# Optimization experiments

Measured on AMD Instinct MI355X. Metric: run time of the kernel, lower is better.

Reference implementation:

```python
import jax, jax.numpy as jnp
import numpy as np

N = 100000
E = 1600000
FEAT = 128
EMB = 64
HID = 64
OUT = 16


def _glorot(key, shape):
    fan_in, fan_out = shape[1], shape[0]
    lim = (6.0 / (fan_in + fan_out)) ** 0.5
    return jax.random.uniform(key, shape, jnp.float32, -lim, lim)


def setup_inputs() -> dict:
    key = jax.random.key(0)
    ks = jax.random.split(key, 16)
    return {
        "x_feat": jax.random.normal(ks[0], (N, FEAT), jnp.float32),
        "x_emb": jax.random.normal(ks[1], (N, 2, EMB), jnp.float32),
        "edge_index": jax.random.randint(ks[2], (2, E), 0, N, jnp.int32),
        # layer 0: SAGEConv(FEAT -> HID), Linear(EMB -> HID)
        "Wl0": _glorot(ks[3], (HID, FEAT)),
        "bl0": jnp.zeros((HID,), jnp.float32),
        "Wr0": _glorot(ks[4], (HID, FEAT)),
        "We0": _glorot(ks[5], (HID, EMB)),
        "be0": jnp.zeros((HID,), jnp.float32),
        # layer 1 (last): SAGEConv(HID -> OUT), Linear(EMB==HID -> OUT)
        "Wl1": _glorot(ks[6], (OUT, HID)),
        "bl1": jnp.zeros((OUT,), jnp.float32),
        "Wr1": _glorot(ks[7], (OUT, HID)),
        "We1": _glorot(ks[8], (OUT, HID)),
        "be1": jnp.zeros((OUT,), jnp.float32),
    }


def _sage_conv(x, edge_index, Wl, bl, Wr):
    # PyG SAGEConv with mean aggregation:
    #   out = lin_l(mean_{j in N(i)} x_j) + lin_r(x_i)
    src, dst = edge_index[0], edge_index[1]
    msg = x[src]                                   # [E, C] gather
    agg = jax.ops.segment_sum(msg, dst, num_segments=N)       # [N, C]
    deg = jax.ops.segment_sum(jnp.ones((E,), x.dtype), dst, num_segments=N)
    agg = agg / jnp.maximum(deg, 1.0)[:, None]     # mean over neighbors
    return agg @ Wl.T + bl + x @ Wr.T


def reference(x_feat, x_emb, edge_index,
              Wl0, bl0, Wr0, We0, be0,
              Wl1, bl1, Wr1, We1, be1):
    # forward(x=(x_feat, x_emb), edge_index=...) path, eval mode (dropout p=0)
    e = x_emb.mean(axis=1)                         # [N, EMB]
    # layer 0 (all but last): relu(sage + linear(emb))
    h = _sage_conv(x_feat, edge_index, Wl0, bl0, Wr0)
    e = e @ We0.T + be0
    h = jax.nn.relu(h + e)
    # last layer: no relu
    h = _sage_conv(h, edge_index, Wl1, bl1, Wr1)
    e = e @ We1.T + be1
    return h + e
```

## Files before the change

### kernel.cpp

```cpp
#include <hip/hip_runtime.h>
#include <hip/hip_bf16.h>
#include <cstddef>

#define NN 100000
#define EE 1600000
#define NPB 128
#define NB  782
#define ECH 4096
#define NCH 391
#define CAP 4096

typedef __attribute__((ext_vector_type(8))) short bf16x8;
typedef __attribute__((ext_vector_type(8))) unsigned short u16x8;
typedef __attribute__((ext_vector_type(4))) float f32x4;

#define YTS 72
#define RTS 68

static inline int ceil_div(int a, int b){ return (a + b - 1) / b; }

__device__ inline unsigned short f2bf(float f){
  union { float f; unsigned u; } v; v.f = f;
  unsigned r = (v.u + 0x7fff + ((v.u >> 16) & 1)) >> 16;
  return (unsigned short)r;
}
__device__ inline float bf2f(unsigned short s){
  union { unsigned u; float f; } v; v.u = ((unsigned)s) << 16;
  return v.f;
}

#define PRE_W (128 * 192)
#define PRE_E (PRE_W + 16 * 64)
#define PRE_B (PRE_E + 16)
#define PRE_C (PRE_B + 64)
#define PRE_N (PRE_C + NB)
__global__ void prep_all_kernel(const float* __restrict__ Wl0, const float* __restrict__ Wr0,
                                const float* __restrict__ We0, const float* __restrict__ bl0,
                                const float* __restrict__ be0, const float* __restrict__ We1,
                                const float* __restrict__ be1,
                                unsigned short* __restrict__ wcat, float* __restrict__ wee,
                                float* __restrict__ b1e, float* __restrict__ bias0,
                                int* __restrict__ cur){
  int idx = blockIdx.x * blockDim.x + threadIdx.x;
  if (idx < PRE_W){
    int n = idx / 192, k = idx % 192;
    float v;
    if (n < 64) v = (k < 128) ? Wl0[n * 128 + k] : 0.f;
    else        v = (k < 128) ? Wr0[(n - 64) * 128 + k] : We0[(n - 64) * 64 + (k - 128)];
    wcat[idx] = f2bf(v);
  } else if (idx < PRE_E){
    int j = idx - PRE_W;
    int i = j >> 6, c = j & 63;
    float s = 0.f;
    for (int k = 0; k < 64; k++) s += We1[i * 64 + k] * We0[k * 64 + c];
    wee[j] = s;
  } else if (idx < PRE_B){
    int i = idx - PRE_E;
    float s = be1[i];
    for (int k = 0; k < 64; k++) s += We1[i * 64 + k] * be0[k];
    b1e[i] = s;
  } else if (idx < PRE_C){
    int i = idx - PRE_B;
    bias0[i] = bl0[i] + be0[i];
  } else if (idx < PRE_N){
    cur[idx - PRE_C] = 0;
  }
}

__global__ void eprep_kernel(const float* __restrict__ xe, unsigned short* __restrict__ eb){
  int g = blockIdx.x * blockDim.x + threadIdx.x;
  if (g >= NN * 8) return;
  int node = g >> 3, q = g & 7;
  float4 a0 = ((const float4*)xe)[(size_t)node * 32 + q * 2];
  float4 a1 = ((const float4*)xe)[(size_t)node * 32 + q * 2 + 1];
  float4 b0 = ((const float4*)xe)[(size_t)node * 32 + 16 + q * 2];
  float4 b1 = ((const float4*)xe)[(size_t)node * 32 + 16 + q * 2 + 1];
  u16x8 o;
  o[0]=f2bf(0.5f*(a0.x+b0.x)); o[1]=f2bf(0.5f*(a0.y+b0.y));
  o[2]=f2bf(0.5f*(a0.z+b0.z)); o[3]=f2bf(0.5f*(a0.w+b0.w));
  o[4]=f2bf(0.5f*(a1.x+b1.x)); o[5]=f2bf(0.5f*(a1.y+b1.y));
  o[6]=f2bf(0.5f*(a1.z+b1.z)); o[7]=f2bf(0.5f*(a1.w+b1.w));
  *(u16x8*)&eb[(size_t)node * 64 + q * 8] = o;
}

__global__ __launch_bounds__(1024) void escatter_kernel(const int* __restrict__ src,
                                                        const int* __restrict__ dst,
                                                        int* __restrict__ cur,
                                                        int* __restrict__ ebkt){
  __shared__ int lh[NB];
  __shared__ int lo[NB];
  const int t = threadIdx.x;
  const int c = blockIdx.x;
  const int e0 = c * ECH;
  int ne = EE - e0; if (ne > ECH) ne = ECH;
  for (int i = t; i < NB; i += 1024) lh[i] = 0;
  __syncthreads();
  int dl[4], sl[4];
  #pragma unroll
  for (int k = 0; k < 4; k++){
    int i = t + k * 1024;
    dl[k] = (i < ne) ? dst[e0 + i] : -1;
    sl[k] = (i < ne) ? src[e0 + i] : 0;
  }
  #pragma unroll
  for (int k = 0; k < 4; k++)
    if (dl[k] >= 0) atomicAdd(&lh[dl[k] >> 7], 1);
  __syncthreads();
  for (int i = t; i < NB; i += 1024){
    int cc = lh[i];
    lo[i] = cc ? atomicAdd(&cur[i], cc) : 0;
    lh[i] = 0;
  }
  __syncthreads();
  #pragma unroll
  for (int k = 0; k < 4; k++){
    if (dl[k] >= 0){
      int d = dl[k], b = d >> 7;
      int r = atomicAdd(&lh[b], 1);
      int p = lo[b] + r;
      if (p < CAP) ebkt[b * CAP + p] = ((d & 127) << 24) | sl[k];
    }
  }
}

__global__ __launch_bounds__(256) void bsort_kernel(
    const int* __restrict__ cur, int* __restrict__ ebkt,
    int* __restrict__ rs, int* __restrict__ deg){
  __shared__ int lraw[CAP];
  __shared__ int lout[CAP];
  __shared__ int lh[NPB];
  __shared__ int loff[NPB];
  __shared__ int lcur[NPB];
  const int t = threadIdx.x;
  const int b = blockIdx.x;
  const int e0 = b * CAP;
  int cnt = cur[b];
  if (cnt > CAP) cnt = CAP;
  for (int i = t; i < NPB; i += 256) lh[i] = 0;
  __syncthreads();
  for (int i = t; i < cnt; i += 256){
    int w = ebkt[e0 + i];
    lraw[i] = w;
    atomicAdd(&lh[((unsigned)w) >> 24], 1);
  }
  __syncthreads();
  {
    int v = (t < NPB) ? lh[t] : 0;
    int s = v;
    for (int off = 1; off < NPB; off <<= 1){
      int x = 0;
      if (t < NPB && t >= off) x = loff[t - off];
      __syncthreads();
      if (t < NPB) loff[t] = s;
      __syncthreads();
      if (t < NPB && t >= off) s += loff[t - off];
      __syncthreads();
    }
    if (t < NPB){ loff[t] = s - v; lcur[t] = s - v; }
  }
  __syncthreads();
  for (int i = t; i < cnt; i += 256){
    int w = lraw[i];
    int d = ((unsigned)w) >> 24;
    int pos = atomicAdd(&lcur[d], 1);
    lout[pos] = w & 0xFFFFFF;
  }
  __syncthreads();
  for (int i = t; i < cnt; i += 256) ebkt[e0 + i] = lout[i];
  if (t < NPB){
    int node = b * NPB + t;
    if (node < NN){
      rs[node]  = e0 + loff[t];
      deg[node] = lh[t];
    }
  }
}

__global__ __launch_bounds__(256, 3) void l0_gemm_kernel(
    const float* __restrict__ xf, const unsigned short* __restrict__ eb,
    const unsigned short* __restrict__ wcat,
    unsigned short* __restrict__ y0g, float* __restrict__ re0g, int M){
  __shared__ unsigned short As[64 * 200];
  __shared__ unsigned short Ys[64 * YTS];
  __shared__ float          Rs[64 * RTS];
  const int t = threadIdx.x;
  const int row0 = blockIdx.x * 64;
  float4 fa[4], fb[4];
  u16x8 ev[2];
  #pragma unroll
  for (int k = 0; k < 4; k++){
    int idx = t + k * 256;
    int r = idx >> 4, o = idx & 15;
    int row = row0 + r;
    if (row < M){
      fa[k] = ((const float4*)xf)[(size_t)row * 32 + o * 2];
      fb[k] = ((const float4*)xf)[(size_t)row * 32 + o * 2 + 1];
    } else {
      fa[k] = make_float4(0.f,0.f,0.f,0.f);
      fb[k] = make_float4(0.f,0.f,0.f,0.f);
    }
  }
  #pragma unroll
  for (int k = 0; k < 2; k++){
    int idx = t + k * 256;
    int r = idx >> 3, q = idx & 7;
    int row = row0 + r;
    u16x8 z = {0,0,0,0,0,0,0,0};
    ev[k] = (row < M) ? *(const u16x8*)&eb[(size_t)row * 64 + q * 8] : z;
  }
  #pragma unroll
  for (int k = 0; k < 4; k++){
    int idx = t + k * 256;
    int r = idx >> 4, o = idx & 15;
    u16x8 ov;
    ov[0]=f2bf(fa[k].x); ov[1]=f2bf(fa[k].y); ov[2]=f2bf(fa[k].z); ov[3]=f2bf(fa[k].w);
    ov[4]=f2bf(fb[k].x); ov[5]=f2bf(fb[k].y); ov[6]=f2bf(fb[k].z); ov[7]=f2bf(fb[k].w);
    *(u16x8*)&As[r * 200 + o * 8] = ov;
  }
  #pragma unroll
  for (int k = 0; k < 2; k++){
    int idx = t + k * 256;
    int r = idx >> 3, q = idx & 7;
    *(u16x8*)&As[r * 200 + 128 + q * 8] = ev[k];
  }
  const int w = t >> 6, l = t & 63;
  const int lm = l & 15, quad = l >> 4;
  bf16x8 bfr0[6], bfr1[6];
  {
    int n0 = w * 16 + lm;
    int n1 = 64 + w * 16 + lm;
    #pragma unroll
    for (int ks = 0; ks < 6; ks++){
      bfr0[ks] = *(const bf16x8*)&wcat[n0 * 192 + ks * 32 + quad * 8];
      bfr1[ks] = *(const bf16x8*)&wcat[n1 * 192 + ks * 32 + quad * 8];
    }
  }
  __syncthreads();
  for (int rg = 0; rg < 4; rg++){
    bf16x8 af[6];
    #pragma unroll
    for (int ks = 0; ks < 6; ks++)
      af[ks] = *(const bf16x8*)&As[(rg * 16 + lm) * 200 + ks * 32 + quad * 8];
    f32x4 acc0 = {0.f, 0.f, 0.f, 0.f};
    f32x4 acc1 = {0.f, 0.f, 0.f, 0.f};
    #pragma unroll
    for (int ks = 0; ks < 6; ks++){
      acc0 = __builtin_amdgcn_mfma_f32_16x16x32_bf16(af[ks], bfr0[ks], acc0, 0, 0, 0);
      acc1 = __builtin_amdgcn_mfma_f32_16x16x32_bf16(af[ks], bfr1[ks], acc1, 0, 0, 0);
    }
    #pragma unroll
    for (int r = 0; r < 4; r++){
      int lrow = rg * 16 + quad * 4 + r;
      Ys[lrow * YTS + w * 16 + lm] = f2bf(acc0[r]);
      Rs[lrow * RTS + w * 16 + lm] = acc1[r];
    }
  }
  __syncthreads();
  #pragma unroll
  for (int k = 0; k < 2; k++){
    int idx = t + k * 256;
    int r = idx >> 3, c8 = idx & 7;
    int grow = row0 + r;
    if (grow < M)
      *(u16x8*)&y0g[(size_t)grow * 64 + c8 * 8] = *(const u16x8*)&Ys[r * YTS + c8 * 8];
  }
  #pragma unroll
  for (int k = 0; k < 4; k++){
    int idx = t + k * 256;
    int r = idx >> 4, c4 = idx & 15;
    int grow = row0 + r;
    if (grow < M)
      *(f32x4*)&re0g[(size_t)grow * 64 + c4 * 4] = *(const f32x4*)&Rs[r * RTS + c4 * 4];
  }
}

__global__ void agg0_kernel(const unsigned short* __restrict__ y0,
                            const float* __restrict__ re0,
                            const float* __restrict__ bias0,
                            const int* __restrict__ rs, const int* __restrict__ deg,
                            const int* __restrict__ ssrc, unsigned short* __restrict__ h){
  int g = blockIdx.x * blockDim.x + threadIdx.x;
  if (g >= NN * 8) return;
  int node = g >> 3, lane = g & 7;
  int start = rs[node], cnt = deg[node];
  float acc[4][8] = {};
  int i = 0;
  for (; i + 8 <= cnt; i += 8){
    int s[8];
    #pragma unroll
    for (int j = 0; j < 8; j++) s[j] = ssrc[start + i + j];
    u16x8 v[8];
    #pragma unroll
    for (int j = 0; j < 8; j++) v[j] = *(const u16x8*)&y0[(size_t)s[j] * 64 + lane * 8];
    #pragma unroll
    for (int j = 0; j < 8; j++)
      #pragma unroll
      for (int k = 0; k < 8; k++) acc[j & 3][k] += bf2f((unsigned short)v[j][k]);
  }
  for (; i < cnt; i++){
    int s = ssrc[start + i];
    u16x8 v = *(const u16x8*)&y0[(size_t)s * 64 + lane * 8];
    #pragma unroll
    for (int k = 0; k < 8; k++) acc[0][k] += bf2f((unsigned short)v[k]);
  }
  float inv = 1.0f / (float)(cnt > 1 ? cnt : 1);
  f32x4 rv0 = *(const f32x4*)&re0[(size_t)node * 64 + lane * 8];
  f32x4 rv1 = *(const f32x4*)&re0[(size_t)node * 64 + lane * 8 + 4];
  float rvv[8] = {rv0[0], rv0[1], rv0[2], rv0[3], rv1[0], rv1[1], rv1[2], rv1[3]};
  float4 ba = ((const float4*)bias0)[lane * 2];
  float4 bb = ((const float4*)bias0)[lane * 2 + 1];
  float bv[8] = {ba.x, ba.y, ba.z, ba.w, bb.x, bb.y, bb.z, bb.w};
  u16x8 o;
  #pragma unroll
  for (int k = 0; k < 8; k++){
    float sum = (acc[0][k] + acc[1][k]) + (acc[2][k] + acc[3][k]);
    float x = sum * inv + rvv[k] + bv[k];
    o[k] = f2bf(x > 0.f ? x : 0.f);
  }
  *(u16x8*)&h[(size_t)node * 64 + lane * 8] = o;
}

__global__ __launch_bounds__(256) void gemm16_dual_kernel(
    const unsigned short* __restrict__ H, const unsigned short* __restrict__ eb,
    const float* __restrict__ Wl1, const float* __restrict__ Wr1,
    const float* __restrict__ wee,
    const float* __restrict__ bl1, const float* __restrict__ b1e,
    unsigned short* __restrict__ Y1, float* __restrict__ Out, int M){
  __shared__ float Hs[64][65];
  __shared__ float Es[64][65];
  __shared__ float Wls[16][65];
  __shared__ float Wrs[16][65];
  __shared__ float Wes[16][65];
  __shared__ float bs[16];
  const int t = threadIdx.x;
  const int row0 = blockIdx.x * 64;
  {
    int j = t >> 4, kq = t & 15;
    float4 a = ((const float4*)Wl1)[j * 16 + kq];
    float4 b = ((const float4*)Wr1)[j * 16 + kq];
    float4 c = ((const float4*)wee)[j * 16 + kq];
    Wls[j][kq*4+0]=a.x; Wls[j][kq*4+1]=a.y; Wls[j][kq*4+2]=a.z; Wls[j][kq*4+3]=a.w;
    Wrs[j][kq*4+0]=b.x; Wrs[j][kq*4+1]=b.y; Wrs[j][kq*4+2]=b.z; Wrs[j][kq*4+3]=b.w;
    Wes[j][kq*4+0]=c.x; Wes[j][kq*4+1]=c.y; Wes[j][kq*4+2]=c.z; Wes[j][kq*4+3]=c.w;
  }
  if (t < 16) bs[t] = bl1[t] + b1e[t];
  for (int idx = t; idx < 64 * 16; idx += 256){
    int n = idx >> 4, kq = idx & 15;
    int row = row0 + n;
    ushort4 hv = make_ushort4(0,0,0,0), evv = make_ushort4(0,0,0,0);
    if (row < M){
      hv  = *(const ushort4*)&H[(size_t)row * 64 + kq * 4];
      evv = *(const ushort4*)&eb[(size_t)row * 64 + kq * 4];
    }
    Hs[n][kq*4+0]=bf2f(hv.x); Hs[n][kq*4+1]=bf2f(hv.y); Hs[n][kq*4+2]=bf2f(hv.z); Hs[n][kq*4+3]=bf2f(hv.w);
    Es[n][kq*4+0]=bf2f(evv.x); Es[n][kq*4+1]=bf2f(evv.y); Es[n][kq*4+2]=bf2f(evv.z); Es[n][kq*4+3]=bf2f(evv.w);
  }
  __syncthreads();
  const int n = t >> 2, jq = t & 3;
  float y[4] = {}, o[4] = {};
  #pragma unroll 4
  for (int k = 0; k < 64; k++){
    float a = Hs[n][k];
    float e = Es[n][k];
    #pragma unroll
    for (int j = 0; j < 4; j++){
      y[j] = fmaf(a, Wls[jq*4 + j][k], y[j]);
      o[j] = fmaf(a, Wrs[jq*4 + j][k], o[j]);
      o[j] = fmaf(e, Wes[jq*4 + j][k], o[j]);
    }
  }
  int row = row0 + n;
  if (row < M){
    ushort4 yb; yb.x = f2bf(y[0]); yb.y = f2bf(y[1]); yb.z = f2bf(y[2]); yb.w = f2bf(y[3]);
    *(ushort4*)&Y1[(size_t)row * 16 + jq * 4] = yb;
    ((float4*)Out)[(size_t)row * 4 + jq] =
        make_float4(o[0] + bs[jq*4+0], o[1] + bs[jq*4+1], o[2] + bs[jq*4+2], o[3] + bs[jq*4+3]);
  }
}

__global__ void agg1_kernel(const unsigned short* __restrict__ y1,
                            const int* __restrict__ rs, const int* __restrict__ deg,
                            const int* __restrict__ ssrc, float* __restrict__ outp){
  int g = blockIdx.x * blockDim.x + threadIdx.x;
  if (g >= NN * 2) return;
  int node = g >> 1, lane = g & 1;
  int start = rs[node], cnt = deg[node];
  float acc[4][8] = {};
  int i = 0;
  for (; i + 8 <= cnt; i += 8){
    int s[8];
    #pragma unroll
    for (int j = 0; j < 8; j++) s[j] = ssrc[start + i + j];
    u16x8 v[8];
    #pragma unroll
    for (int j = 0; j < 8; j++) v[j] = *(const u16x8*)&y1[(size_t)s[j] * 16 + lane * 8];
    #pragma unroll
    for (int j = 0; j < 8; j++)
      #pragma unroll
      for (int k = 0; k < 8; k++) acc[j & 3][k] += bf2f((unsigned short)v[j][k]);
  }
  for (; i < cnt; i++){
    int s = ssrc[start + i];
    u16x8 v = *(const u16x8*)&y1[(size_t)s * 16 + lane * 8];
    #pragma unroll
    for (int k = 0; k < 8; k++) acc[0][k] += bf2f((unsigned short)v[k]);
  }
  float inv = 1.0f / (float)(cnt > 1 ? cnt : 1);
  f32x4 o0 = *(f32x4*)&outp[(size_t)node * 16 + lane * 8];
  f32x4 o1 = *(f32x4*)&outp[(size_t)node * 16 + lane * 8 + 4];
  #pragma unroll
  for (int k = 0; k < 4; k++){
    o0[k] += ((acc[0][k] + acc[1][k]) + (acc[2][k] + acc[3][k])) * inv;
    o1[k] += ((acc[0][k+4] + acc[1][k+4]) + (acc[2][k+4] + acc[3][k+4])) * inv;
  }
  *(f32x4*)&outp[(size_t)node * 16 + lane * 8]     = o0;
  *(f32x4*)&outp[(size_t)node * 16 + lane * 8 + 4] = o1;
}

extern "C" void kernel_launch(void* const* d_in, const int* in_sizes, int n_in,
                              void* d_out, int out_size, void* d_ws, size_t ws_size,
                              hipStream_t stream){
  (void)in_sizes; (void)n_in; (void)out_size; (void)ws_size;
  const float* x_feat = (const float*)d_in[0];
  const float* x_emb  = (const float*)d_in[1];
  const int*   ei     = (const int*)d_in[2];
  const float* Wl0 = (const float*)d_in[3];
  const float* bl0 = (const float*)d_in[4];
  const float* Wr0 = (const float*)d_in[5];
  const float* We0 = (const float*)d_in[6];
  const float* be0 = (const float*)d_in[7];
  const float* Wl1 = (const float*)d_in[8];
  const float* bl1 = (const float*)d_in[9];
  const float* Wr1 = (const float*)d_in[10];
  const float* We1 = (const float*)d_in[11];
  const float* be1 = (const float*)d_in[12];
  float* out = (float*)d_out;

  char* w = (char*)d_ws;
  float* re0          = (float*)w;           w += sizeof(float) * (size_t)NN * 64;
  unsigned short* y0  = (unsigned short*)w;  w += sizeof(unsigned short) * (size_t)NN * 64;
  unsigned short* eb  = (unsigned short*)w;  w += sizeof(unsigned short) * (size_t)NN * 64;
  unsigned short* h   = (unsigned short*)w;  w += sizeof(unsigned short) * (size_t)NN * 64;
  unsigned short* y1  = (unsigned short*)w;  w += sizeof(unsigned short) * (size_t)NN * 16;
  unsigned short* wcat= (unsigned short*)w;  w += sizeof(unsigned short) * 128 * 192;
  float* wee   = (float*)w;                  w += sizeof(float) * 16 * 64;
  float* b1e   = (float*)w;                  w += sizeof(float) * 16;
  float* bias0 = (float*)w;                  w += sizeof(float) * 64;
  int* ebkt    = (int*)w;                    w += sizeof(int) * (size_t)NB * CAP;
  int* cur     = (int*)w;                    w += sizeof(int) * NB;
  int* rs      = (int*)w;                    w += sizeof(int) * NN;
  int* deg     = (int*)w;                    w += sizeof(int) * NN;

  const int* srcp = ei;
  const int* dstp = ei + EE;

  prep_all_kernel<<<ceil_div(PRE_N, 256), 256, 0, stream>>>(
      Wl0, Wr0, We0, bl0, be0, We1, be1, wcat, wee, b1e, bias0, cur);

  escatter_kernel<<<NCH, 1024, 0, stream>>>(srcp, dstp, cur, ebkt);
  bsort_kernel<<<NB, 256, 0, stream>>>(cur, ebkt, rs, deg);

  eprep_kernel<<<ceil_div(NN * 8, 256), 256, 0, stream>>>(x_emb, eb);

  l0_gemm_kernel<<<ceil_div(NN, 64), 256, 0, stream>>>(x_feat, eb, wcat, y0, re0, NN);

  agg0_kernel<<<ceil_div(NN * 8, 256), 256, 0, stream>>>(
      y0, re0, bias0, rs, deg, ebkt, h);

  gemm16_dual_kernel<<<ceil_div(NN, 64), 256, 0, stream>>>(h, eb, Wl1, Wr1, wee,
                                                           bl1, b1e, y1, out, NN);
  agg1_kernel<<<ceil_div(NN * 2, 256), 256, 0, stream>>>(y1, rs, deg, ebkt, out);
}
```

Before: 282.8 us.

## Fuse bucket sort into layer-0 aggregation kernel using shared-memory sorted edges

Removes the separate bucket-sort kernel and performs the per-bucket counting sort inside the layer-0 aggregation kernel, one block per 128-node bucket. Neighbor indices are then read from shared memory instead of global memory, and one launch is saved. The sorted edges, rs and deg are still written out for the layer-1 aggregation. In exchange, the aggregation now runs on only 782 blocks with 32KB of shared memory each, which lowers occupancy and parallelism for the gather-heavy phase.

```diff
diff --git a/kernel.cpp b/kernel.cpp
--- a/kernel.cpp
+++ b/kernel.cpp
@@ -123,59 +123,6 @@
   }
 }
 
-__global__ __launch_bounds__(256) void bsort_kernel(
-    const int* __restrict__ cur, int* __restrict__ ebkt,
-    int* __restrict__ rs, int* __restrict__ deg){
-  __shared__ int lraw[CAP];
-  __shared__ int lout[CAP];
-  __shared__ int lh[NPB];
-  __shared__ int loff[NPB];
-  __shared__ int lcur[NPB];
-  const int t = threadIdx.x;
-  const int b = blockIdx.x;
-  const int e0 = b * CAP;
-  int cnt = cur[b];
-  if (cnt > CAP) cnt = CAP;
-  for (int i = t; i < NPB; i += 256) lh[i] = 0;
-  __syncthreads();
-  for (int i = t; i < cnt; i += 256){
-    int w = ebkt[e0 + i];
-    lraw[i] = w;
-    atomicAdd(&lh[((unsigned)w) >> 24], 1);
-  }
-  __syncthreads();
-  {
-    int v = (t < NPB) ? lh[t] : 0;
-    int s = v;
-    for (int off = 1; off < NPB; off <<= 1){
-      int x = 0;
-      if (t < NPB && t >= off) x = loff[t - off];
-      __syncthreads();
-      if (t < NPB) loff[t] = s;
-      __syncthreads();
-      if (t < NPB && t >= off) s += loff[t - off];
-      __syncthreads();
-    }
-    if (t < NPB){ loff[t] = s - v; lcur[t] = s - v; }
-  }
-  __syncthreads();
-  for (int i = t; i < cnt; i += 256){
-    int w = lraw[i];
-    int d = ((unsigned)w) >> 24;
-    int pos = atomicAdd(&lcur[d], 1);
-    lout[pos] = w & 0xFFFFFF;
-  }
-  __syncthreads();
-  for (int i = t; i < cnt; i += 256) ebkt[e0 + i] = lout[i];
-  if (t < NPB){
-    int node = b * NPB + t;
-    if (node < NN){
-      rs[node]  = e0 + loff[t];
-      deg[node] = lh[t];
-    }
-  }
-}
-
 __global__ __launch_bounds__(256, 3) void l0_gemm_kernel(
     const float* __restrict__ xf, const unsigned short* __restrict__ eb,
     const unsigned short* __restrict__ wcat,
@@ -274,50 +221,98 @@
   }
 }
 
-__global__ void agg0_kernel(const unsigned short* __restrict__ y0,
-                            const float* __restrict__ re0,
-                            const float* __restrict__ bias0,
-                            const int* __restrict__ rs, const int* __restrict__ deg,
-                            const int* __restrict__ ssrc, unsigned short* __restrict__ h){
-  int g = blockIdx.x * blockDim.x + threadIdx.x;
-  if (g >= NN * 8) return;
-  int node = g >> 3, lane = g & 7;
-  int start = rs[node], cnt = deg[node];
-  float acc[4][8] = {};
-  int i = 0;
-  for (; i + 8 <= cnt; i += 8){
-    int s[8];
-    #pragma unroll
-    for (int j = 0; j < 8; j++) s[j] = ssrc[start + i + j];
-    u16x8 v[8];
-    #pragma unroll
-    for (int j = 0; j < 8; j++) v[j] = *(const u16x8*)&y0[(size_t)s[j] * 64 + lane * 8];
-    #pragma unroll
-    for (int j = 0; j < 8; j++)
+__global__ __launch_bounds__(256) void agg0_kernel(
+    const unsigned short* __restrict__ y0, const float* __restrict__ re0,
+    const float* __restrict__ bias0, const int* __restrict__ cur,
+    int* __restrict__ ebkt, int* __restrict__ rs, int* __restrict__ deg,
+    unsigned short* __restrict__ h){
+  __shared__ int lraw[CAP];
+  __shared__ int lsrt[CAP];
+  __shared__ int lh[NPB];
+  __shared__ int loff[NPB];
+  __shared__ int lcur[NPB];
+  const int t = threadIdx.x;
+  const int b = blockIdx.x;
+  const int e0 = b * CAP;
+  int cnt = cur[b]; if (cnt > CAP) cnt = CAP;
+  for (int i = t; i < NPB; i += 256) lh[i] = 0;
+  __syncthreads();
+  for (int i = t; i < cnt; i += 256){
+    int w = ebkt[e0 + i];
+    lraw[i] = w;
+    atomicAdd(&lh[((unsigned)w) >> 24], 1);
+  }
+  __syncthreads();
+  {
+    int v = (t < NPB) ? lh[t] : 0;
+    int s = v;
+    for (int off = 1; off < NPB; off <<= 1){
+      __syncthreads();
+      if (t < NPB) loff[t] = s;
+      __syncthreads();
+      if (t < NPB && t >= off) s += loff[t - off];
+    }
+    __syncthreads();
+    if (t < NPB){ loff[t] = s - v; lcur[t] = s - v; }
+  }
+  __syncthreads();
+  for (int i = t; i < cnt; i += 256){
+    int w = lraw[i];
+    int d = ((unsigned)w) >> 24;
+    int pos = atomicAdd(&lcur[d], 1);
+    lsrt[pos] = w & 0xFFFFFF;
+  }
+  __syncthreads();
+  for (int i = t; i < cnt; i += 256) ebkt[e0 + i] = lsrt[i];
+  if (t < NPB){
+    int node = b * NPB + t;
+    if (node < NN){
+      rs[node]  = e0 + loff[t];
+      deg[node] = lh[t];
+    }
+  }
+  const int lane = t & 7;
+  for (int sub = 0; sub < 4; sub++){
+    int r = sub * 32 + (t >> 3);
+    int node = b * NPB + r;
+    if (node >= NN) continue;
+    int start = loff[r], cn = lh[r];
+    float acc[4][8] = {};
+    int i = 0;
+    for (; i + 8 <= cn; i += 8){
+      int s[8];
       #pragma unroll
-      for (int k = 0; k < 8; k++) acc[j & 3][k] += bf2f((unsigned short)v[j][k]);
-  }
-  for (; i < cnt; i++){
-    int s = ssrc[start + i];
-    u16x8 v = *(const u16x8*)&y0[(size_t)s * 64 + lane * 8];
-    #pragma unroll
-    for (int k = 0; k < 8; k++) acc[0][k] += bf2f((unsigned short)v[k]);
-  }
-  float inv = 1.0f / (float)(cnt > 1 ? cnt : 1);
-  f32x4 rv0 = *(const f32x4*)&re0[(size_t)node * 64 + lane * 8];
-  f32x4 rv1 = *(const f32x4*)&re0[(size_t)node * 64 + lane * 8 + 4];
-  float rvv[8] = {rv0[0], rv0[1], rv0[2], rv0[3], rv1[0], rv1[1], rv1[2], rv1[3]};
-  float4 ba = ((const float4*)bias0)[lane * 2];
-  float4 bb = ((const float4*)bias0)[lane * 2 + 1];
-  float bv[8] = {ba.x, ba.y, ba.z, ba.w, bb.x, bb.y, bb.z, bb.w};
-  u16x8 o;
-  #pragma unroll
-  for (int k = 0; k < 8; k++){
-    float sum = (acc[0][k] + acc[1][k]) + (acc[2][k] + acc[3][k]);
-    float x = sum * inv + rvv[k] + bv[k];
-    o[k] = f2bf(x > 0.f ? x : 0.f);
-  }
-  *(u16x8*)&h[(size_t)node * 64 + lane * 8] = o;
+      for (int j = 0; j < 8; j++) s[j] = lsrt[start + i + j];
+      u16x8 v[8];
+      #pragma unroll
+      for (int j = 0; j < 8; j++) v[j] = *(const u16x8*)&y0[(size_t)s[j] * 64 + lane * 8];
+      #pragma unroll
+      for (int j = 0; j < 8; j++)
+        #pragma unroll
+        for (int k = 0; k < 8; k++) acc[j & 3][k] += bf2f((unsigned short)v[j][k]);
+    }
+    for (; i < cn; i++){
+      int s = lsrt[start + i];
+      u16x8 v = *(const u16x8*)&y0[(size_t)s * 64 + lane * 8];
+      #pragma unroll
+      for (int k = 0; k < 8; k++) acc[0][k] += bf2f((unsigned short)v[k]);
+    }
+    float inv = 1.0f / (float)(cn > 1 ? cn : 1);
+    f32x4 rv0 = *(const f32x4*)&re0[(size_t)node * 64 + lane * 8];
+    f32x4 rv1 = *(const f32x4*)&re0[(size_t)node * 64 + lane * 8 + 4];
+    float rvv[8] = {rv0[0], rv0[1], rv0[2], rv0[3], rv1[0], rv1[1], rv1[2], rv1[3]};
+    float4 ba = ((const float4*)bias0)[lane * 2];
+    float4 bb = ((const float4*)bias0)[lane * 2 + 1];
+    float bv[8] = {ba.x, ba.y, ba.z, ba.w, bb.x, bb.y, bb.z, bb.w};
+    u16x8 o;
+    #pragma unroll
+    for (int k = 0; k < 8; k++){
+      float sum = (acc[0][k] + acc[1][k]) + (acc[2][k] + acc[3][k]);
+      float x = sum * inv + rvv[k] + bv[k];
+      o[k] = f2bf(x > 0.f ? x : 0.f);
+    }
+    *(u16x8*)&h[(size_t)node * 64 + lane * 8] = o;
+  }
 }
 
 __global__ __launch_bounds__(256) void gemm16_dual_kernel(
@@ -458,14 +453,12 @@
       Wl0, Wr0, We0, bl0, be0, We1, be1, wcat, wee, b1e, bias0, cur);
 
   escatter_kernel<<<NCH, 1024, 0, stream>>>(srcp, dstp, cur, ebkt);
-  bsort_kernel<<<NB, 256, 0, stream>>>(cur, ebkt, rs, deg);
 
   eprep_kernel<<<ceil_div(NN * 8, 256), 256, 0, stream>>>(x_emb, eb);
 
   l0_gemm_kernel<<<ceil_div(NN, 64), 256, 0, stream>>>(x_feat, eb, wcat, y0, re0, NN);
 
-  agg0_kernel<<<ceil_div(NN * 8, 256), 256, 0, stream>>>(
-      y0, re0, bias0, rs, deg, ebkt, h);
+  agg0_kernel<<<NB, 256, 0, stream>>>(y0, re0, bias0, cur, ebkt, rs, deg, h);
 
   gemm16_dual_kernel<<<ceil_div(NN, 64), 256, 0, stream>>>(h, eb, Wl1, Wr1, wee,
                                                            bl1, b1e, y1, out, NN);
```

After: 272.3 us. 3.7% less time.
